# Kernel optimization log

Measured on AMD Instinct MI355X. Metric: run time of the kernel, lower is better.

## Reference

```python
import jax, jax.numpy as jnp
import numpy as np

N, F_IN, D_IN, D_OUT = 1024, 256, 128, 64  # nodes, raw feat, in_features, out_features


def setup_inputs() -> dict:
    key = jax.random.key(0)
    k_adj, k_x, k_lw, k_w = jax.random.split(key, 4)
    # Random symmetric binary adjacency, avg degree ~32, self-loops on the diagonal
    p = 32.0 / N
    u = jax.random.uniform(k_adj, (N, N))
    A = (u < p).astype(jnp.float32)
    A = jnp.maximum(A, A.T)
    diag = jnp.arange(N)
    A = A.at[diag, diag].set(1.0)
    # --- caculation(): derived masks ---
    A0 = A.at[diag, diag].set(0.0)                 # adjacency without self loops
    sib = A0 @ A0 + A0                             # sibling matrix
    sib = sib.at[diag, diag].set(0.0)
    neighbor_count = jnp.maximum(A0.sum(axis=1, keepdims=True), 1.0)  # [N,1]
    # --- features and parameters ---
    node_features = jax.random.normal(k_x, (N, F_IN), dtype=jnp.float32)
    k_lw1, k_lw2 = jax.random.split(k_lw)
    lin_w = jax.random.normal(k_lw1, (D_IN, F_IN), dtype=jnp.float32) * np.float32(np.sqrt(2.0 / F_IN))
    lin_b = jnp.zeros((D_IN,), dtype=jnp.float32)
    weight = jax.random.normal(k_w, (D_IN, D_OUT), dtype=jnp.float32) * np.float32(np.sqrt(2.0 / D_IN))
    return {
        "node_features": node_features,
        "adjacency_matrix": A,
        "mask_father": A[:, None, :],              # [N,1,N]
        "neighbor_count": neighbor_count,          # [N,1]
        "mask_hadamard": sib[:, None, :],          # [N,1,N]
        "lin_w": lin_w,
        "lin_b": lin_b,
        "weight": weight,
    }


def reference(node_features, adjacency_matrix, mask_father, neighbor_count, mask_hadamard, lin_w, lin_b, weight):
    # Linear projection created inside torch forward: x @ W^T + b
    x = node_features @ lin_w.T + lin_b            # [N, D_IN]
    wf = x @ weight                                # [N, F]  (F = out_features)
    sib = mask_hadamard[:, 0, :]                   # [N, N]
    mf = mask_father[:, 0, :]                      # [N, N]
    # H[b,f,j] = wf[b,f] * wf[j,f] * sib[b,j]   (masked pairwise hadamard, [N,F,N])
    H = wf[:, :, None] * wf.T[None, :, :] * sib[:, None, :]
    # S[i,f,j] = sum_b A[i,b] * H[b,f,j]        (batched adjacency matmul)
    S = jnp.einsum('ib,bfj->ifj', adjacency_matrix, H)
    # mask by father adjacency, sum over j, normalize by neighbor_count^2
    out = (S * mf[:, None, :]).sum(axis=2) / (neighbor_count ** 2)   # [N, F]
    return out
```

## Files before the change

### kernel.cpp

```cpp
#include <hip/hip_runtime.h>

#define N 1024
#define F_IN 256
#define D_IN 128
#define D_OUT 64
#define KMAX 128

__global__ __launch_bounds__(256) void prep_w2_kernel(
    const float* __restrict__ A, const float* __restrict__ sib,
    const float* __restrict__ lin_w, const float* __restrict__ lin_b,
    const float* __restrict__ weight,
    unsigned char* __restrict__ sib8, unsigned short* __restrict__ nbrg,
    int* __restrict__ cntg, float* __restrict__ W2, float* __restrict__ b2)
{
    const int t = threadIdx.x;
    if (blockIdx.x >= N) {
        const int blk = blockIdx.x - N;
        if (blk < 64) {
            const int k = blk * 4 + (t >> 6);
            const int f = t & 63;
            float acc = 0.0f;
            #pragma unroll 4
            for (int d = 0; d < D_IN; ++d)
                acc += lin_w[d * F_IN + k] * weight[d * D_OUT + f];
            W2[k * D_OUT + f] = acc;
        } else if (t < D_OUT) {
            float acc = 0.0f;
            #pragma unroll 4
            for (int d = 0; d < D_IN; ++d)
                acc += lin_b[d] * weight[d * D_OUT + t];
            b2[t] = acc;
        }
        return;
    }

    const int i = blockIdx.x;
    const int lane = t & 63, wave = t >> 6;

    {
        const float4 v = ((const float4*)(sib + (size_t)i * N))[t];
        uchar4 u;
        u.x = (unsigned char)(v.x + 0.5f);
        u.y = (unsigned char)(v.y + 0.5f);
        u.z = (unsigned char)(v.z + 0.5f);
        u.w = (unsigned char)(v.w + 0.5f);
        ((uchar4*)(sib8 + (size_t)i * N))[t] = u;
    }

    __shared__ int woff[4];
    __shared__ int base;
    if (t == 0) base = 0;
    const float* arow = A + (size_t)i * N;
    for (int c = 0; c < 4; ++c) {
        __syncthreads();
        const int j = c * 256 + t;
        const float a = arow[j];
        const unsigned long long m = __ballot(a != 0.0f);
        if (lane == 0) woff[wave] = __popcll(m);
        __syncthreads();
        int off = base;
        for (int w = 0; w < wave; ++w) off += woff[w];
        const int pos = off + __popcll(m & ((1ULL << lane) - 1ULL));
        if (a != 0.0f && pos < KMAX) nbrg[(size_t)i * KMAX + pos] = (unsigned short)j;
        __syncthreads();
        if (t == 0) base += woff[0] + woff[1] + woff[2] + woff[3];
    }
    __syncthreads();
    if (t == 0) cntg[i] = base < KMAX ? base : KMAX;
}

__global__ __launch_bounds__(256) void wf2_kernel(
    const float* __restrict__ nf, const float* __restrict__ W2,
    const float* __restrict__ b2, float* __restrict__ wf)
{
    __shared__ float red[4 * D_OUT];
    const int t = threadIdx.x, lane = t & 63, wave = t >> 6;
    const int row = blockIdx.x * 2 + (wave >> 1);
    const int half = wave & 1;
    const float4* nf4 = (const float4*)(nf + (size_t)row * F_IN);
    float acc = half ? 0.0f : b2[lane];
    #pragma unroll 8
    for (int kk = half * 32; kk < half * 32 + 32; ++kk) {
        const float4 v = nf4[kk];
        const float* w = W2 + kk * 4 * D_OUT + lane;
        acc += v.x * w[0] + v.y * w[D_OUT] + v.z * w[2 * D_OUT] + v.w * w[3 * D_OUT];
    }
    red[wave * D_OUT + lane] = acc;
    __syncthreads();
    if (t < 128) {
        const int rr = t >> 6, f = t & 63;
        wf[(size_t)(blockIdx.x * 2 + rr) * D_OUT + f] =
            red[(rr * 2) * D_OUT + f] + red[(rr * 2 + 1) * D_OUT + f];
    }
}

__global__ __launch_bounds__(1024, 8) void pair2_kernel(
    const unsigned char* __restrict__ sib8, const unsigned short* __restrict__ nbrg,
    const int* __restrict__ cntg, const float* __restrict__ nc,
    const float* __restrict__ wf, float* __restrict__ out)
{
    __shared__ float          wf_s[(KMAX + 4) * D_OUT];
    __shared__ unsigned char  sib_s[KMAX * KMAX];
    __shared__ unsigned short nbr[KMAX];
    __shared__ float          red[16 * D_OUT];

    const int i = blockIdx.x, t = threadIdx.x;
    const int wave = t >> 6, lane = t & 63;
    int K = cntg[i]; if (K > 124) K = 124;

    if (t < 512) {
        const int bi = t >> 2;
        sib_s[bi * KMAX + K + (t & 3)] = 0;
    } else if (t < 768) {
        wf_s[K * D_OUT + (t - 512)] = 0.0f;
    }
    if (t < KMAX) nbr[t] = nbrg[(size_t)i * KMAX + t];
    __syncthreads();

    for (int idx = t; idx < K * (D_OUT / 4); idx += 1024)
        ((float4*)wf_s)[idx] =
            ((const float4*)wf)[(int)nbr[idx >> 4] * (D_OUT / 4) + (idx & 15)];
    for (int idx = t; idx < K * KMAX; idx += 1024) {
        const int bi = idx >> 7, j = idx & (KMAX - 1);
        if (j > bi && j < K) sib_s[idx] = sib8[(size_t)nbr[bi] * N + nbr[j]];
    }
    __syncthreads();

    const int f4 = (lane & 15) * 4, p = lane >> 4;
    float4 acc = make_float4(0.f, 0.f, 0.f, 0.f);
    for (int bi = wave; bi < K; bi += 16) {
        const float4 wb = *(const float4*)&wf_s[bi * D_OUT + f4];
        const unsigned char* sr = sib_s + bi * KMAX;
        for (int j0 = bi + 1; j0 < K; j0 += 4) {
            const int j = j0 + p;
            const float s = (float)sr[j];
            const float4 wj = *(const float4*)&wf_s[j * D_OUT + f4];
            acc.x += s * (wb.x * wj.x);
            acc.y += s * (wb.y * wj.y);
            acc.z += s * (wb.z * wj.z);
            acc.w += s * (wb.w * wj.w);
        }
    }
    #pragma unroll
    for (int m = 16; m <= 32; m += m) {
        acc.x += __shfl_xor(acc.x, m, 64);
        acc.y += __shfl_xor(acc.y, m, 64);
        acc.z += __shfl_xor(acc.z, m, 64);
        acc.w += __shfl_xor(acc.w, m, 64);
    }
    if (p == 0) *(float4*)&red[wave * D_OUT + f4] = acc;
    __syncthreads();

    if (t < D_OUT) {
        float v = 0.f;
        #pragma unroll
        for (int w = 0; w < 16; ++w) v += red[w * D_OUT + t];
        const float c = nc[i];
        out[(size_t)i * D_OUT + t] = 2.0f * v / (c * c);
    }
}

extern "C" void kernel_launch(void* const* d_in, const int* in_sizes, int n_in,
                              void* d_out, int out_size, void* d_ws, size_t ws_size,
                              hipStream_t stream) {
    const float* nf     = (const float*)d_in[0];
    const float* A      = (const float*)d_in[1];
    const float* nc     = (const float*)d_in[3];
    const float* sib    = (const float*)d_in[4];
    const float* lin_w  = (const float*)d_in[5];
    const float* lin_b  = (const float*)d_in[6];
    const float* weight = (const float*)d_in[7];
    float*       out    = (float*)d_out;

    char* ws = (char*)d_ws;
    float*          wf    = (float*)(ws);
    float*          W2    = (float*)(ws + 262144);
    float*          b2    = (float*)(ws + 327680);
    unsigned char*  sib8  = (unsigned char*)(ws + 328704);
    unsigned short* nbr16 = (unsigned short*)(ws + 1377280);
    int*            cnt   = (int*)(ws + 1639424);

    prep_w2_kernel<<<N + 65, 256,  0, stream>>>(A, sib, lin_w, lin_b, weight,
                                                sib8, nbr16, cnt, W2, b2);
    wf2_kernel    <<<N / 2,  256,  0, stream>>>(nf, W2, b2, wf);
    pair2_kernel  <<<N,      1024, 0, stream>>>(sib8, nbr16, cnt, nc, wf, out);
}
```

Before: 113.4 us.

## Block pair loop by four rows with transposed sibling tile

Transposes the shared sibling tile (padded row stride) so each wave handles four consecutive b rows at once and reads a uchar4 of sibling values per j. Each wf_s[j] load is reused across four b rows instead of one. This cuts LDS traffic and loop overhead in the pairwise accumulation. In exchange, the whole sibling tile is zeroed up front and triangle blocks are padded, so some extra zero-weighted work is done near the diagonal.

```diff
diff --git a/kernel.cpp b/kernel.cpp
--- a/kernel.cpp
+++ b/kernel.cpp
@@ -5,6 +5,7 @@
 #define D_IN 128
 #define D_OUT 64
 #define KMAX 128
+#define SROW 132
 
 __global__ __launch_bounds__(256) void prep_w2_kernel(
     const float* __restrict__ A, const float* __restrict__ sib,
@@ -100,7 +101,7 @@
     const float* __restrict__ wf, float* __restrict__ out)
 {
     __shared__ float          wf_s[(KMAX + 4) * D_OUT];
-    __shared__ unsigned char  sib_s[KMAX * KMAX];
+    __shared__ unsigned char  sib_sT[KMAX * SROW];
     __shared__ unsigned short nbr[KMAX];
     __shared__ float          red[16 * D_OUT];
 
@@ -108,12 +109,9 @@
     const int wave = t >> 6, lane = t & 63;
     int K = cntg[i]; if (K > 124) K = 124;
 
-    if (t < 512) {
-        const int bi = t >> 2;
-        sib_s[bi * KMAX + K + (t & 3)] = 0;
-    } else if (t < 768) {
-        wf_s[K * D_OUT + (t - 512)] = 0.0f;
-    }
+    for (int idx = t; idx < (KMAX * SROW) / 16; idx += 1024)
+        ((int4*)sib_sT)[idx] = make_int4(0, 0, 0, 0);
+    if (t < 256) wf_s[K * D_OUT + t] = 0.0f;
     if (t < KMAX) nbr[t] = nbrg[(size_t)i * KMAX + t];
     __syncthreads();
 
@@ -122,23 +120,34 @@
             ((const float4*)wf)[(int)nbr[idx >> 4] * (D_OUT / 4) + (idx & 15)];
     for (int idx = t; idx < K * KMAX; idx += 1024) {
         const int bi = idx >> 7, j = idx & (KMAX - 1);
-        if (j > bi && j < K) sib_s[idx] = sib8[(size_t)nbr[bi] * N + nbr[j]];
+        if (j > bi && j < K)
+            sib_sT[j * SROW + bi] = sib8[(size_t)nbr[bi] * N + nbr[j]];
     }
     __syncthreads();
 
     const int f4 = (lane & 15) * 4, p = lane >> 4;
     float4 acc = make_float4(0.f, 0.f, 0.f, 0.f);
-    for (int bi = wave; bi < K; bi += 16) {
-        const float4 wb = *(const float4*)&wf_s[bi * D_OUT + f4];
-        const unsigned char* sr = sib_s + bi * KMAX;
-        for (int j0 = bi + 1; j0 < K; j0 += 4) {
+    for (int bt = wave; bt * 4 < K; bt += 16) {
+        const float4 wb0 = *(const float4*)&wf_s[(bt * 4 + 0) * D_OUT + f4];
+        const float4 wb1 = *(const float4*)&wf_s[(bt * 4 + 1) * D_OUT + f4];
+        const float4 wb2 = *(const float4*)&wf_s[(bt * 4 + 2) * D_OUT + f4];
+        const float4 wb3 = *(const float4*)&wf_s[(bt * 4 + 3) * D_OUT + f4];
+        const unsigned char* sc = sib_sT + bt * 4;
+        for (int j0 = bt * 4; j0 < K; j0 += 4) {
             const int j = j0 + p;
-            const float s = (float)sr[j];
+            const uchar4 s4 = *(const uchar4*)(sc + j * SROW);
             const float4 wj = *(const float4*)&wf_s[j * D_OUT + f4];
-            acc.x += s * (wb.x * wj.x);
-            acc.y += s * (wb.y * wj.y);
-            acc.z += s * (wb.z * wj.z);
-            acc.w += s * (wb.w * wj.w);
+            const float sx = (float)s4.x, sy = (float)s4.y,
+                        sz = (float)s4.z, sw = (float)s4.w;
+            float4 u;
+            u.x = sx * wb0.x + sy * wb1.x + sz * wb2.x + sw * wb3.x;
+            u.y = sx * wb0.y + sy * wb1.y + sz * wb2.y + sw * wb3.y;
+            u.z = sx * wb0.z + sy * wb1.z + sz * wb2.z + sw * wb3.z;
+            u.w = sx * wb0.w + sy * wb1.w + sz * wb2.w + sw * wb3.w;
+            acc.x += u.x * wj.x;
+            acc.y += u.y * wj.y;
+            acc.z += u.z * wj.z;
+            acc.w += u.w * wj.w;
         }
     }
     #pragma unroll
```

After: 106.9 us (median of 2 runs). 5.7% less time.
